# Kernel tuning notes

Hardware: AMD Instinct MI355X
Metric: run time of the kernel (lower is better)

## Reference

```python
import jax, jax.numpy as jnp
import numpy as np
import math

B = 2048
INPUT_SIZE = 1024
OUTPUT_SIZE = 512
SPONGE = 1024
ACT = 256
REC = 256
STORE = ACT + REC  # 512
DEPTH = 8
BDEPTH = 10
NEUTRAL_C = 1.0
SQRT2 = math.sqrt(2.0)


def _make_structure():
    # Deterministic stand-in for the module's random.sample-based recall wiring.
    rng = np.random.RandomState(0)
    half = (SPONGE + 1) // 2
    shuffle_perm = np.array([i // 2 + (i % 2) * half for i in range(SPONGE)], dtype=np.int64)
    unused = []
    recall = []
    for i in range(DEPTH):
        unused.extend(range(i * STORE, (i + 1) * STORE))
        sel = rng.choice(len(unused), size=REC, replace=False)
        sel_set = set(sel.tolist())
        recall.append([unused[k] for k in sorted(sel_set)])
        unused = [u for k, u in enumerate(unused) if k not in sel_set]
    out_mem = np.array(sorted(unused), dtype=np.int64)  # 2048 leftover memory columns
    bf_size = len(out_mem) + SPONGE  # 3072
    bf_depth = int(math.ceil(math.log2(bf_size)))  # 12
    bf_half = (bf_size + 1) // 2
    bf_perm = np.array([i // 2 + (i % 2) * bf_half for i in range(bf_size)], dtype=np.int64)
    return shuffle_perm, np.array(recall, dtype=np.int64), out_mem, bf_perm, bf_size, bf_depth


def setup_inputs() -> dict:
    key = jax.random.key(0)
    ks = jax.random.split(key, 6)
    shuffle_perm, recall_idx, out_mem_idx, bf_perm, bf_size, bf_depth = _make_structure()
    return {
        "X": jax.random.normal(ks[0], (B, INPUT_SIZE), jnp.float32),
        "scales": jnp.ones((INPUT_SIZE,), jnp.float32),
        "angles": jax.random.uniform(ks[1], (DEPTH, BDEPTH, SPONGE // 2), jnp.float32) * (2 * math.pi),
        "act_bias": jax.random.normal(ks[2], (DEPTH, ACT), jnp.float32),
        "act_activation": jax.random.normal(ks[3], (DEPTH, ACT), jnp.float32),
        "act_curvature": jax.random.normal(ks[4], (DEPTH, ACT), jnp.float32),
        "bf_angles": jax.random.uniform(ks[5], (bf_depth, bf_size // 2), jnp.float32) * (2 * math.pi),
        "shuffle_perm": jnp.asarray(shuffle_perm),
        "recall_idx": jnp.asarray(recall_idx),
        "output_mem_idx": jnp.asarray(out_mem_idx),
        "bf_perm": jnp.asarray(bf_perm),
    }


def _base_activation(x, c):
    # In the source, `a` is overwritten with torch.tensor(1.0), so a == 1.
    t = (math.pi / 4) / c
    y0 = (1.0 / c) * (1.0 / SQRT2 - math.cos(math.pi / 2))  # = 1/(c*sqrt(2))
    m0 = math.sin(math.pi / 2)  # = 1
    y1 = (1.0 / c) * (1.0 / SQRT2 - 1.0)
    m1 = math.sin(0.0)  # = 0
    mid = (1.0 / c) * (1.0 / SQRT2 - jnp.cos(math.pi / 4 + c * x))
    return jnp.where(x > t, y0 + m0 * (x - t), jnp.where(x < -t, y1 + m1 * (x + t), mid))


def _butterfly(x, angles, perm):
    # angles: [n_layers, exch]; shuffle -> Givens rotation per pair, extra passthrough
    exch = angles.shape[1]
    for j in range(angles.shape[0]):
        s = x[:, perm]
        x1, x2 = s[:, :exch], s[:, exch:2 * exch]
        ca, sa = jnp.cos(angles[j]), jnp.sin(angles[j])
        x = jnp.concatenate([ca * x1 + sa * x2, -sa * x1 + ca * x2, s[:, 2 * exch:]], axis=1)
    return x


def reference(X, scales, angles, act_bias, act_activation, act_curvature, bf_angles,
              shuffle_perm, recall_idx, output_mem_idx, bf_perm):
    Xs = X * scales
    sponge = Xs[:, :SPONGE]  # input_size == sponge_size: no zero pad, memory[0] is empty
    mem = jnp.zeros((Xs.shape[0], DEPTH * STORE), Xs.dtype)
    for i in range(DEPTH):
        sponge = _butterfly(sponge, angles[i], shuffle_perm)
        x1 = sponge[:, STORE:STORE + ACT] + act_bias[i]  # activation_position == store_size
        c = 0.5 * NEUTRAL_C * (act_curvature[i] + jnp.sqrt(act_curvature[i] ** 2 + 1.0))
        ap = _base_activation(x1, c)
        am = _base_activation(-x1, c)
        act_out = jnp.stack([ap, am], axis=2).reshape(ap.shape[0], 2 * ACT)  # interleave +/-
        mem = mem.at[:, i * STORE:(i + 1) * STORE].set(sponge[:, :STORE])
        recall = mem[:, recall_idx[i]]  # indices only address already-filled columns
        # [act_out | sponge[store:act_pos] (empty) | sponge[act_pos+ACT:] | recall]
        sponge = jnp.concatenate([act_out, sponge[:, STORE + ACT:], recall], axis=1)
    pre = jnp.concatenate([mem[:, output_mem_idx], sponge], axis=1)  # [B, 3072]
    out = _butterfly(pre, bf_angles, bf_perm)
    return out[:, :OUTPUT_SIZE]
```

## Files before the change

### kernel.cpp

```cpp
#include <hip/hip_runtime.h>
#include <math.h>

#define NB 2048
#define DEPTH 8

#define FTAB_OFF    0
#define BF01_OFF    81920
#define BFF_OFF     88064
#define ACT4_OFF    98304
#define PHYSA_OFF   106496
#define PHYSR_OFF   110592
#define PHYSO2_OFF  112640

__global__ void setup_kernel(const float* __restrict__ angles,
                             const float* __restrict__ bf_angles,
                             const float* __restrict__ act_bias,
                             const float* __restrict__ act_curv,
                             const int* __restrict__ recall_idx,
                             const int* __restrict__ out_mem_idx,
                             float* __restrict__ ws) {
    __shared__ int physL[4096];
    if (blockIdx.x < 200) {
        int id = blockIdx.x * 256 + threadIdx.x;
        if (id < 40960) {
            int w = id & 3, t = (id >> 2) & 255, dg = id >> 10;
            int d = dg / 5, g = dg - 5 * d;
            int a = 2 * (t & 127) + (t >> 7);
            int pair = (w == 0) ? a : (w == 1) ? (a + 256)
                     : (w == 2) ? (2 * a) : (2 * a + 1);
            int st = 2 * g + (w >> 1);
            float ang = angles[(d * 10 + st) * 512 + pair];
            float s, c; sincosf(ang, &s, &c);
            ws[FTAB_OFF + 2 * id]     = c;
            ws[FTAB_OFF + 2 * id + 1] = s;
        } else if (id < 44032) {
            int e = id - 40960;
            int w = e & 3; int ti = e >> 2;
            int t = ti / 3; int i = ti - 3 * t;
            int a = t + 256 * i;
            int pair = (w == 0) ? a : (w == 1) ? (a + 768)
                     : (w == 2) ? (2 * a) : (2 * a + 1);
            int stage = (w < 2) ? 0 : 1;
            float ang = bf_angles[stage * 1536 + pair];
            float s, c; sincosf(ang, &s, &c);
            ws[BF01_OFF + 2 * e]     = c;
            ws[BF01_OFF + 2 * e + 1] = s;
        } else if (id < 49152) {
            int e = id - 44032;
            int f = e >> 10; int rem = e & 1023; int t = rem >> 2; int w = rem & 3;
            int P;
            if (f == 0) P = 3 * t;
            else if (f < 4) { int k = 8 - 2 * f;
                              P = ((t >> (2 * f)) * (768 >> k)) + (t & ((256 >> k) - 1)); }
            else P = t;
            int pair = (w == 0) ? P : (w == 1) ? (P + 768)
                     : (w == 2) ? (2 * P) : (2 * P + 1);
            int stage = (w < 2) ? (2 + 2 * f) : (3 + 2 * f);
            float ang = bf_angles[stage * 1536 + pair];
            float s, c; sincosf(ang, &s, &c);
            ws[BFF_OFF + 2 * e]     = c;
            ws[BFF_OFF + 2 * e + 1] = s;
        } else if (id < 51200) {
            int ida = id - 49152;
            float cu = act_curv[ida];
            float c  = 0.5f * (cu + sqrtf(cu * cu + 1.0f));
            ((float4*)(ws + ACT4_OFF))[ida] =
                make_float4(act_bias[ida], c, 1.0f / c, 0.0f);
        }
    } else {
        int tid = threadIdx.x;
        for (int e = tid; e < 4096; e += 256) {
            int v = e, p;
            for (;;) {
                int d = v >> 9, j = v & 511;
                if (d == 0)  { p = j; break; }
                if (j < 256) { p = 256 + d * 256 + j; break; }
                v = recall_idx[(d - 1) * 256 + (j - 256)];
            }
            physL[e] = p;
        }
        __syncthreads();
        int* pa = (int*)(ws + PHYSA_OFF);
        for (int e = tid; e < 2048; e += 256) {
            int d = e >> 8, t = e & 255;
            int a = 2 * (t & 127) + (t >> 7);
            pa[2 * e]     = physL[d * 512 + 2 * a];
            pa[2 * e + 1] = physL[d * 512 + 2 * a + 1];
        }
        int* pr = (int*)(ws + PHYSR_OFF);
        for (int e = tid; e < 2048; e += 256)
            pr[e] = physL[recall_idx[e]];
        int* po = (int*)(ws + PHYSO2_OFF);
        for (int e = tid; e < 3072; e += 256) {
            int tt = e / 12; int r = e - 12 * tt; int i = r >> 2; int k = r & 3;
            int a = tt + 256 * i;
            int tl2 = a >> 1, th2 = a & 1;
            int pos = tl2 + 1536 * th2 + 384 * k;
            po[e] = (pos < 2048) ? physL[out_mem_idx[pos]] : 2304 + (pos - 2048);
        }
    }
}

__device__ __forceinline__ float actf(float x, float c, float ic) {
    const float is2 = 0.70710678118654752f;
    float tt = 0.78539816339744831f * ic;
    float y0 = is2 * ic;
    float y1 = (is2 - 1.0f) * ic;
    float mid = ic * (is2 - __cosf(0.78539816339744831f + c * x));
    return x > tt ? (y0 + (x - tt)) : (x < -tt ? y1 : mid);
}

__device__ __forceinline__ int xf(int A) { return A ^ (((A >> 7) & 1) << 2); }

__launch_bounds__(256, 4)
__global__ void sponge_kernel(const float* __restrict__ X,
                              const float* __restrict__ scales,
                              const float* __restrict__ ws,
                              float* __restrict__ out) {
    __shared__ float lds[8704];
    float* L0 = lds;
    float* L1 = lds + 4352;
    const int t = threadIdx.x;
    const int rowA = blockIdx.x * 2;

    const float4* bf01  = (const float4*)(ws + BF01_OFF);
    const float4* bff   = (const float4*)(ws + BFF_OFF);
    const float4* act4  = (const float4*)(ws + ACT4_OFF);
    const int2* physA  = (const int2*)(ws + PHYSA_OFF);
    const int*  physr  = (const int*)(ws + PHYSR_OFF);
    const int*  physo2 = (const int*)(ws + PHYSO2_OFF);

    const int tl = t & 127, th = t >> 7;
    const int b  = tl + th * 512;
    const int a  = 2 * tl + th;

    const int wq = xf(4 * a);
    const int rb = xf(4 * (tl >> 1) + (tl & 1) + 2 * th);
    const int u  = t - 128;
    int za0 = 0, za1 = 0, za2 = 0, za3 = 0, kb = 0;
    if (t < 128) {
        int k0 = t >> 1;
        int zb = 4 * (k0 >> 1) + (k0 & 1) + 2;
        za0 = xf(zb); za1 = xf(zb + 128); za2 = xf(zb + 256); za3 = xf(zb + 384);
    } else {
        kb = xf(512 + 4 * (u >> 1) + 2 + (u & 1));
    }

    float hA0, hA1, hA2, hA3, hB0, hB1, hB2, hB3;
    {
        const float* Xr0 = X + (size_t)rowA * 1024;
        const float* Xr1 = Xr0 + 1024;
        float s0 = scales[b], s1 = scales[b + 128];
        float s2 = scales[b + 256], s3 = scales[b + 384];
        hA0 = Xr0[b] * s0; hA1 = Xr0[b + 128] * s1;
        hA2 = Xr0[b + 256] * s2; hA3 = Xr0[b + 384] * s3;
        hB0 = Xr1[b] * s0; hB1 = Xr1[b + 128] * s1;
        hB2 = Xr1[b + 256] * s2; hB3 = Xr1[b + 384] * s3;
    }

    int woff = 2304, roff = 3328;
    const float4* ft = (const float4*)(ws + FTAB_OFF) + 2 * t;

#define DQUAD(cA, cB, i0, i1, i2, i3, F0, F1, F2, F3)                    \
    { float g0 =  (cA).x * (i0) + (cA).y * (i2);                         \
      float g2 = -(cA).y * (i0) + (cA).x * (i2);                         \
      float g1 =  (cA).z * (i1) + (cA).w * (i3);                         \
      float g3 = -(cA).w * (i1) + (cA).z * (i3);                         \
      F0 =  (cB).x * g0 + (cB).y * g1;                                   \
      F2 = -(cB).y * g0 + (cB).x * g1;                                   \
      F1 =  (cB).z * g2 + (cB).w * g3;                                   \
      F3 = -(cB).w * g2 + (cB).z * g3; }

    for (int d = 0; d < DEPTH; ++d) {
        for (int g = 0; g < 5; ++g) {
            float4 csA = ft[0], csB = ft[1]; ft += 512;
            float fA0, fA1, fA2, fA3, fB0, fB1, fB2, fB3;
            DQUAD(csA, csB, hA0, hA1, hA2, hA3, fA0, fA1, fA2, fA3);
            DQUAD(csA, csB, hB0, hB1, hB2, hB3, fB0, fB1, fB2, fB3);
            if (g < 4) {
                *(float4*)(L0 + woff + wq) = make_float4(fA0, fA1, fA2, fA3);
                *(float4*)(L1 + woff + wq) = make_float4(fB0, fB1, fB2, fB3);
                { int tmp = woff; woff = roff; roff = tmp; }
                __syncthreads();
                const float* e0 = L0 + roff + rb;
                const float* e1 = L1 + roff + rb;
                hA0 = e0[0]; hA1 = e0[256]; hA2 = e0[512]; hA3 = e0[768];
                hB0 = e1[0]; hB1 = e1[256]; hB2 = e1[512]; hB3 = e1[768];
            } else {
                int2 pm = physA[d * 256 + t];
                L0[pm.x] = fA0; L0[pm.y] = fA1;
                L1[pm.x] = fB0; L1[pm.y] = fB1;
                *(float2*)(L0 + woff + wq + 2) = make_float2(fA2, fA3);
                *(float2*)(L1 + woff + wq + 2) = make_float2(fB2, fB3);
                { int tmp = woff; woff = roff; roff = tmp; }
                int r0 = 0, r1 = 0;
                float4 a0, a1, a2, a3;
                if (t < 128) {
                    int k0 = t >> 1;
                    a0 = act4[d * 256 + k0];
                    a1 = act4[d * 256 + k0 + 64];
                    a2 = act4[d * 256 + k0 + 128];
                    a3 = act4[d * 256 + k0 + 192];
                } else {
                    r0 = physr[d * 256 + u];
                    r1 = physr[d * 256 + u + 128];
                }
                __syncthreads();
                const float* z0 = L0 + roff;
                const float* z1 = L1 + roff;
                if (t < 128) {
                    float sgn = (t & 1) ? -1.0f : 1.0f;
                    hA0 = actf(sgn * (z0[za0] + a0.x), a0.y, a0.z);
                    hA1 = actf(sgn * (z0[za1] + a1.x), a1.y, a1.z);
                    hA2 = actf(sgn * (z0[za2] + a2.x), a2.y, a2.z);
                    hA3 = actf(sgn * (z0[za3] + a3.x), a3.y, a3.z);
                    hB0 = actf(sgn * (z1[za0] + a0.x), a0.y, a0.z);
                    hB1 = actf(sgn * (z1[za1] + a1.x), a1.y, a1.z);
                    hB2 = actf(sgn * (z1[za2] + a2.x), a2.y, a2.z);
                    hB3 = actf(sgn * (z1[za3] + a3.x), a3.y, a3.z);
                } else {
                    hA0 = z0[kb]; hA1 = z0[kb + 256];
                    hB0 = z1[kb]; hB1 = z1[kb + 256];
                    hA2 = L0[r0]; hA3 = L0[r1];
                    hB2 = L1[r0]; hB3 = L1[r1];
                }
            }
        }
    }

    L0[2304 + b] = hA0; L0[2304 + b + 128] = hA1;
    L0[2304 + b + 256] = hA2; L0[2304 + b + 384] = hA3;
    L1[2304 + b] = hB0; L1[2304 + b + 128] = hB1;
    L1[2304 + b + 256] = hB2; L1[2304 + b + 384] = hB3;
    __syncthreads();

    float vA0, vA1, vA2, vA3, vA4, vA5, vA6, vA7, vA8, vA9, vA10, vA11;
    float vB0, vB1, vB2, vB3, vB4, vB5, vB6, vB7, vB8, vB9, vB10, vB11;
    {
        int4 pg = ((const int4*)(physo2 + t * 12))[0];
        vA0 = L0[pg.x]; vA1 = L0[pg.y]; vA2 = L0[pg.z]; vA3 = L0[pg.w];
        vB0 = L1[pg.x]; vB1 = L1[pg.y]; vB2 = L1[pg.z]; vB3 = L1[pg.w];
        pg = ((const int4*)(physo2 + t * 12))[1];
        vA4 = L0[pg.x]; vA5 = L0[pg.y]; vA6 = L0[pg.z]; vA7 = L0[pg.w];
        vB4 = L1[pg.x]; vB5 = L1[pg.y]; vB6 = L1[pg.z]; vB7 = L1[pg.w];
        pg = ((const int4*)(physo2 + t * 12))[2];
        vA8 = L0[pg.x]; vA9 = L0[pg.y]; vA10 = L0[pg.z]; vA11 = L0[pg.w];
        vB8 = L1[pg.x]; vB9 = L1[pg.y]; vB10 = L1[pg.z]; vB11 = L1[pg.w];
    }
    __syncthreads();

#define BF01_STEP(i, qA0, qA1, qA2, qA3, qB0, qB1, qB2, qB3)                        \
    {                                                                               \
        float4 c01 = bf01[(t * 3 + (i)) * 2];                                       \
        float4 c23 = bf01[(t * 3 + (i)) * 2 + 1];                                   \
        float y0, y1, y2, y3;                                                       \
        DQUAD(c01, c23, qA0, qA1, qA2, qA3, y0, y1, y2, y3);                        \
        *(float2*)(L0 + 2 * t + 512 * (i))        = make_float2(y0, y1);            \
        *(float2*)(L0 + 2 * t + 512 * (i) + 1536) = make_float2(y2, y3);            \
        DQUAD(c01, c23, qB0, qB1, qB2, qB3, y0, y1, y2, y3);                        \
        *(float2*)(L1 + 2 * t + 512 * (i))        = make_float2(y0, y1);            \
        *(float2*)(L1 + 2 * t + 512 * (i) + 1536) = make_float2(y2, y3);            \
    }
    BF01_STEP(0, vA0, vA1, vA2, vA3, vB0, vB1, vB2, vB3)
    BF01_STEP(1, vA4, vA5, vA6, vA7, vB4, vB5, vB6, vB7)
    BF01_STEP(2, vA8, vA9, vA10, vA11, vB8, vB9, vB10, vB11)
#undef BF01_STEP
    __syncthreads();

#pragma unroll
    for (int f = 0; f < 4; ++f) {
        int P;
        if (f == 0) P = 3 * t;
        else { const int k = 8 - 2 * f;
               P = ((t >> (2 * f)) * (768 >> k)) + (t & ((256 >> k) - 1)); }
        int base = (P >> 1) + (P & 1) * 1536;
        float4 csS = bff[(f * 256 + t) * 2];
        float4 csT = bff[(f * 256 + t) * 2 + 1];
        float xA1p = L0[base], xA1q = L0[base + 384];
        float xA2p = L0[base + 768], xA2q = L0[base + 1152];
        float xB1p = L1[base], xB1q = L1[base + 384];
        float xB2p = L1[base + 768], xB2q = L1[base + 1152];
        float o1P =  csS.x * xA1p + csS.y * xA2p;
        float o2P = -csS.y * xA1p + csS.x * xA2p;
        float o1Q =  csS.z * xA1q + csS.w * xA2q;
        float o2Q = -csS.w * xA1q + csS.z * xA2q;
        float yA0 =  csT.x * o1P + csT.y * o1Q;
        float yA2 = -csT.y * o1P + csT.x * o1Q;
        float yA1 =  csT.z * o2P + csT.w * o2Q;
        float yA3 = -csT.w * o2P + csT.z * o2Q;
        o1P =  csS.x * xB1p + csS.y * xB2p;
        o2P = -csS.y * xB1p + csS.x * xB2p;
        o1Q =  csS.z * xB1q + csS.w * xB2q;
        o2Q = -csS.w * xB1q + csS.z * xB2q;
        float yB0 =  csT.x * o1P + csT.y * o1Q;
        float yB2 = -csT.y * o1P + csT.x * o1Q;
        float yB1 =  csT.z * o2P + csT.w * o2Q;
        float yB3 = -csT.w * o2P + csT.z * o2Q;
        __syncthreads();
        *(float2*)(L0 + 2 * P)        = make_float2(yA0, yA1);
        *(float2*)(L0 + 2 * P + 1536) = make_float2(yA2, yA3);
        *(float2*)(L1 + 2 * P)        = make_float2(yB0, yB1);
        *(float2*)(L1 + 2 * P + 1536) = make_float2(yB2, yB3);
        __syncthreads();
    }

    {
        int base = (t >> 1) + (t & 1) * 1536;
        float4 csS = bff[(4 * 256 + t) * 2];
        float4 csT = bff[(4 * 256 + t) * 2 + 1];
        float x1p = L0[base], x1q = L0[base + 384];
        float x2p = L0[base + 768], x2q = L0[base + 1152];
        float o1P =  csS.x * x1p + csS.y * x2p;
        float o2P = -csS.y * x1p + csS.x * x2p;
        float o1Q =  csS.z * x1q + csS.w * x2q;
        float o2Q = -csS.w * x1q + csS.z * x2q;
        *(float2*)(out + (size_t)rowA * 512 + 2 * t) =
            make_float2(csT.x * o1P + csT.y * o1Q, csT.z * o2P + csT.w * o2Q);
        x1p = L1[base]; x1q = L1[base + 384];
        x2p = L1[base + 768]; x2q = L1[base + 1152];
        o1P =  csS.x * x1p + csS.y * x2p;
        o2P = -csS.y * x1p + csS.x * x2p;
        o1Q =  csS.z * x1q + csS.w * x2q;
        o2Q = -csS.w * x1q + csS.z * x2q;
        *(float2*)(out + (size_t)(rowA + 1) * 512 + 2 * t) =
            make_float2(csT.x * o1P + csT.y * o1Q, csT.z * o2P + csT.w * o2Q);
    }
#undef DQUAD
}

extern "C" void kernel_launch(void* const* d_in, const int* in_sizes, int n_in,
                              void* d_out, int out_size, void* d_ws, size_t ws_size,
                              hipStream_t stream) {
    const float* X          = (const float*)d_in[0];
    const float* scales     = (const float*)d_in[1];
    const float* angles     = (const float*)d_in[2];
    const float* act_bias   = (const float*)d_in[3];
    const float* act_curv   = (const float*)d_in[5];
    const float* bf_angles  = (const float*)d_in[6];
    const int*   recall_idx  = (const int*)d_in[8];
    const int*   out_mem_idx = (const int*)d_in[9];

    float* ws = (float*)d_ws;

    setup_kernel<<<201, 256, 0, stream>>>(angles, bf_angles, act_bias, act_curv,
                                          recall_idx, out_mem_idx, ws);
    sponge_kernel<<<NB / 2, 256, 0, stream>>>(X, scales, ws, (float*)d_out);
}
```

Before: 122.3 us.

## Remap thread-to-element assignment and LDS swizzle in sponge butterfly stages

Changes how the 256 threads map onto the 1024 sponge elements. The old layout had half-warp splits and an XOR swizzle on bit 7; the new one interleaves even and odd threads, writes float2 pairs with a new XOR swizzle on bits 5-6, and splits the activation and recall work by thread parity instead of by thread half. The precomputed angle and physical-index tables in setup are updated to match. The aim is fewer LDS bank conflicts and more balanced wave work in the activation step, at the cost of float4 LDS writes becoming pairs of float2 writes.

```diff
diff --git a/kernel.cpp b/kernel.cpp
--- a/kernel.cpp
+++ b/kernel.cpp
@@ -25,7 +25,7 @@
         if (id < 40960) {
             int w = id & 3, t = (id >> 2) & 255, dg = id >> 10;
             int d = dg / 5, g = dg - 5 * d;
-            int a = 2 * (t & 127) + (t >> 7);
+            int a = t;
             int pair = (w == 0) ? a : (w == 1) ? (a + 256)
                      : (w == 2) ? (2 * a) : (2 * a + 1);
             int st = 2 * g + (w >> 1);
@@ -83,9 +83,8 @@
         int* pa = (int*)(ws + PHYSA_OFF);
         for (int e = tid; e < 2048; e += 256) {
             int d = e >> 8, t = e & 255;
-            int a = 2 * (t & 127) + (t >> 7);
-            pa[2 * e]     = physL[d * 512 + 2 * a];
-            pa[2 * e + 1] = physL[d * 512 + 2 * a + 1];
+            pa[2 * e]     = physL[d * 512 + 2 * t];
+            pa[2 * e + 1] = physL[d * 512 + 2 * t + 1];
         }
         int* pr = (int*)(ws + PHYSR_OFF);
         for (int e = tid; e < 2048; e += 256)
@@ -110,7 +109,7 @@
     return x > tt ? (y0 + (x - tt)) : (x < -tt ? y1 : mid);
 }
 
-__device__ __forceinline__ int xf(int A) { return A ^ (((A >> 7) & 1) << 2); }
+__device__ __forceinline__ int fld(int s) { return s ^ (((s >> 5) & 3) << 3); }
 
 __launch_bounds__(256, 4)
 __global__ void sponge_kernel(const float* __restrict__ X,
@@ -130,32 +129,20 @@
     const int*  physr  = (const int*)(ws + PHYSR_OFF);
     const int*  physo2 = (const int*)(ws + PHYSO2_OFF);
 
-    const int tl = t & 127, th = t >> 7;
-    const int b  = tl + th * 512;
-    const int a  = 2 * tl + th;
-
-    const int wq = xf(4 * a);
-    const int rb = xf(4 * (tl >> 1) + (tl & 1) + 2 * th);
-    const int u  = t - 128;
-    int za0 = 0, za1 = 0, za2 = 0, za3 = 0, kb = 0;
-    if (t < 128) {
-        int k0 = t >> 1;
-        int zb = 4 * (k0 >> 1) + (k0 & 1) + 2;
-        za0 = xf(zb); za1 = xf(zb + 128); za2 = xf(zb + 256); za3 = xf(zb + 384);
-    } else {
-        kb = xf(512 + 4 * (u >> 1) + 2 + (u & 1));
-    }
+    const int bq = (t >> 1) + 512 * (t & 1);
+    const int W0 = fld(((2 * t) & 127) + 256 * (t >> 6));
+    const int rb = fld((t >> 1) + 128 * (t & 1));
 
     float hA0, hA1, hA2, hA3, hB0, hB1, hB2, hB3;
     {
         const float* Xr0 = X + (size_t)rowA * 1024;
         const float* Xr1 = Xr0 + 1024;
-        float s0 = scales[b], s1 = scales[b + 128];
-        float s2 = scales[b + 256], s3 = scales[b + 384];
-        hA0 = Xr0[b] * s0; hA1 = Xr0[b + 128] * s1;
-        hA2 = Xr0[b + 256] * s2; hA3 = Xr0[b + 384] * s3;
-        hB0 = Xr1[b] * s0; hB1 = Xr1[b + 128] * s1;
-        hB2 = Xr1[b + 256] * s2; hB3 = Xr1[b + 384] * s3;
+        float s0 = scales[bq],       s1 = scales[bq + 128];
+        float s2 = scales[bq + 256], s3 = scales[bq + 384];
+        hA0 = Xr0[bq] * s0; hA1 = Xr0[bq + 128] * s1;
+        hA2 = Xr0[bq + 256] * s2; hA3 = Xr0[bq + 384] * s3;
+        hB0 = Xr1[bq] * s0; hB1 = Xr1[bq + 128] * s1;
+        hB2 = Xr1[bq + 256] * s2; hB3 = Xr1[bq + 384] * s3;
     }
 
     int woff = 2304, roff = 3328;
@@ -178,8 +165,10 @@
             DQUAD(csA, csB, hA0, hA1, hA2, hA3, fA0, fA1, fA2, fA3);
             DQUAD(csA, csB, hB0, hB1, hB2, hB3, fB0, fB1, fB2, fB3);
             if (g < 4) {
-                *(float4*)(L0 + woff + wq) = make_float4(fA0, fA1, fA2, fA3);
-                *(float4*)(L1 + woff + wq) = make_float4(fB0, fB1, fB2, fB3);
+                *(float2*)(L0 + woff + W0)       = make_float2(fA0, fA1);
+                *(float2*)(L0 + woff + W0 + 128) = make_float2(fA2, fA3);
+                *(float2*)(L1 + woff + W0)       = make_float2(fB0, fB1);
+                *(float2*)(L1 + woff + W0 + 128) = make_float2(fB2, fB3);
                 { int tmp = woff; woff = roff; roff = tmp; }
                 __syncthreads();
                 const float* e0 = L0 + roff + rb;
@@ -190,37 +179,39 @@
                 int2 pm = physA[d * 256 + t];
                 L0[pm.x] = fA0; L0[pm.y] = fA1;
                 L1[pm.x] = fB0; L1[pm.y] = fB1;
-                *(float2*)(L0 + woff + wq + 2) = make_float2(fA2, fA3);
-                *(float2*)(L1 + woff + wq + 2) = make_float2(fB2, fB3);
+                *(float2*)(L0 + woff + 2 * t) = make_float2(fA2, fA3);
+                *(float2*)(L1 + woff + 2 * t) = make_float2(fB2, fB3);
                 { int tmp = woff; woff = roff; roff = tmp; }
                 int r0 = 0, r1 = 0;
                 float4 a0, a1, a2, a3;
-                if (t < 128) {
-                    int k0 = t >> 1;
-                    a0 = act4[d * 256 + k0];
-                    a1 = act4[d * 256 + k0 + 64];
-                    a2 = act4[d * 256 + k0 + 128];
-                    a3 = act4[d * 256 + k0 + 192];
+                if (!(t & 1)) {
+                    int kk = t >> 2;
+                    a0 = act4[d * 256 + kk];
+                    a1 = act4[d * 256 + kk + 64];
+                    a2 = act4[d * 256 + kk + 128];
+                    a3 = act4[d * 256 + kk + 192];
                 } else {
-                    r0 = physr[d * 256 + u];
-                    r1 = physr[d * 256 + u + 128];
+                    r0 = physr[d * 256 + (t >> 1)];
+                    r1 = physr[d * 256 + (t >> 1) + 128];
                 }
                 __syncthreads();
-                const float* z0 = L0 + roff;
-                const float* z1 = L1 + roff;
-                if (t < 128) {
-                    float sgn = (t & 1) ? -1.0f : 1.0f;
-                    hA0 = actf(sgn * (z0[za0] + a0.x), a0.y, a0.z);
-                    hA1 = actf(sgn * (z0[za1] + a1.x), a1.y, a1.z);
-                    hA2 = actf(sgn * (z0[za2] + a2.x), a2.y, a2.z);
-                    hA3 = actf(sgn * (z0[za3] + a3.x), a3.y, a3.z);
-                    hB0 = actf(sgn * (z1[za0] + a0.x), a0.y, a0.z);
-                    hB1 = actf(sgn * (z1[za1] + a1.x), a1.y, a1.z);
-                    hB2 = actf(sgn * (z1[za2] + a2.x), a2.y, a2.z);
-                    hB3 = actf(sgn * (z1[za3] + a3.x), a3.y, a3.z);
+                const float* Z0 = L0 + roff;
+                const float* Z1 = L1 + roff;
+                if (!(t & 1)) {
+                    int kk = t >> 2;
+                    float sgn = (t & 2) ? -1.0f : 1.0f;
+                    hA0 = actf(sgn * (Z0[kk]       + a0.x), a0.y, a0.z);
+                    hA1 = actf(sgn * (Z0[kk + 64]  + a1.x), a1.y, a1.z);
+                    hA2 = actf(sgn * (Z0[kk + 128] + a2.x), a2.y, a2.z);
+                    hA3 = actf(sgn * (Z0[kk + 192] + a3.x), a3.y, a3.z);
+                    hB0 = actf(sgn * (Z1[kk]       + a0.x), a0.y, a0.z);
+                    hB1 = actf(sgn * (Z1[kk + 64]  + a1.x), a1.y, a1.z);
+                    hB2 = actf(sgn * (Z1[kk + 128] + a2.x), a2.y, a2.z);
+                    hB3 = actf(sgn * (Z1[kk + 192] + a3.x), a3.y, a3.z);
                 } else {
-                    hA0 = z0[kb]; hA1 = z0[kb + 256];
-                    hB0 = z1[kb]; hB1 = z1[kb + 256];
+                    int j = t >> 1;
+                    hA0 = Z0[256 + j]; hA1 = Z0[384 + j];
+                    hB0 = Z1[256 + j]; hB1 = Z1[384 + j];
                     hA2 = L0[r0]; hA3 = L0[r1];
                     hB2 = L1[r0]; hB3 = L1[r1];
                 }
@@ -228,10 +219,10 @@
         }
     }
 
-    L0[2304 + b] = hA0; L0[2304 + b + 128] = hA1;
-    L0[2304 + b + 256] = hA2; L0[2304 + b + 384] = hA3;
-    L1[2304 + b] = hB0; L1[2304 + b + 128] = hB1;
-    L1[2304 + b + 256] = hB2; L1[2304 + b + 384] = hB3;
+    L0[2304 + bq] = hA0; L0[2304 + bq + 128] = hA1;
+    L0[2304 + bq + 256] = hA2; L0[2304 + bq + 384] = hA3;
+    L1[2304 + bq] = hB0; L1[2304 + bq + 128] = hB1;
+    L1[2304 + bq + 256] = hB2; L1[2304 + bq + 384] = hB3;
     __syncthreads();
 
     float vA0, vA1, vA2, vA3, vA4, vA5, vA6, vA7, vA8, vA9, vA10, vA11;
```

New measurement: 124.1 us. About the same (+1.5%).
